# Performance work log

Hardware: AMD Instinct MI355X
Metric: run time of the kernel (lower is better)

Reference implementation:

```python
import jax, jax.numpy as jnp
import numpy as np

E = 768
H = 12
D = E // H  # 64


def setup_inputs() -> dict:
    key = jax.random.key(0)
    ks = jax.random.split(key, 12)
    B, S = 4, 2048
    scale = 1.0 / np.sqrt(E)
    inp = {
        "q": jax.random.normal(ks[0], (B, S, E), jnp.float32),
        "k": jax.random.normal(ks[1], (B, S, E), jnp.float32),
        "v": jax.random.normal(ks[2], (B, S, E), jnp.float32),
        "mask": jax.random.randint(ks[3], (B, S), 0, 2, jnp.int32),
        "Wq": jax.random.normal(ks[4], (E, E), jnp.float32) * scale,
        "bq": jnp.zeros((E,), jnp.float32),
        "Wk": jax.random.normal(ks[5], (E, E), jnp.float32) * scale,
        "bk": jnp.zeros((E,), jnp.float32),
        "Wv": jax.random.normal(ks[6], (E, E), jnp.float32) * scale,
        "bv": jnp.zeros((E,), jnp.float32),
        "Wo": jax.random.normal(ks[7], (E, E), jnp.float32) * scale,
        "bo": jnp.zeros((E,), jnp.float32),
    }
    return inp


def reference(q, k, v, mask, Wq, bq, Wk, bk, Wv, bv, Wo, bo):
    B, Sq, _ = q.shape
    Sk = k.shape[1]
    # QKV projections, split into heads: [B, H, S, D]
    qh = (q @ Wq + bq).reshape(B, Sq, H, D).transpose(0, 2, 1, 3)
    kh = (k @ Wk + bk).reshape(B, Sk, H, D).transpose(0, 2, 1, 3)
    vh = (v @ Wv + bv).reshape(B, Sk, H, D).transpose(0, 2, 1, 3)
    scores = jnp.einsum("bhqd,bhkd->bhqk", qh, kh) / jnp.sqrt(jnp.float32(D))
    # enc=True padding-mask path: positions where mask==0 get -1e9 added
    bias = jnp.where(mask == 0, jnp.float32(-1e9), jnp.float32(0.0))  # [B, Sk]
    scores = scores + bias[:, None, None, :]
    weights = jax.nn.softmax(scores, axis=-1)
    # dropout is identity in eval mode
    ctx = jnp.einsum("bhqk,bhkd->bqhd", weights, vh).reshape(B, Sq, E)
    return ctx @ Wo + bo
```

## Files before the change

kernel.cpp:

```cpp
#include <hip/hip_runtime.h>
#include <hip/hip_bf16.h>
#include <stdint.h>


typedef __bf16 bf16x8 __attribute__((ext_vector_type(8)));
typedef __bf16 bf16x4 __attribute__((ext_vector_type(4)));
typedef float floatx4 __attribute__((ext_vector_type(4)));

#define MFMA_BF16(a, b, c) __builtin_amdgcn_mfma_f32_16x16x32_bf16(a, b, c, 0, 0, 0)


__device__ __forceinline__ void glds16(const __bf16* g, __bf16* l) {
  __builtin_amdgcn_global_load_lds(
      (const __attribute__((address_space(1))) unsigned int*)g,
      (__attribute__((address_space(3))) unsigned int*)l, 16, 0, 0);
}

#if __has_builtin(__builtin_amdgcn_permlane32_swap)
__device__ __forceinline__ void perm32_swap(unsigned int& a, unsigned int& b) {
  auto r = __builtin_amdgcn_permlane32_swap(a, b, false, false);
  a = r[0];
  b = r[1];
}
#else
__device__ __forceinline__ void perm32_swap(unsigned int& a, unsigned int& b) {
  asm("v_permlane32_swap_b32 %0, %1" : "+v"(a), "+v"(b));
}
#endif

#if __has_builtin(__builtin_amdgcn_permlane16_swap)
__device__ __forceinline__ void perm16_swap(unsigned int& a, unsigned int& b) {
  auto r = __builtin_amdgcn_permlane16_swap(a, b, false, false);
  a = r[0];
  b = r[1];
}
#else
__device__ __forceinline__ void perm16_swap(unsigned int& a, unsigned int& b) {
  asm("v_permlane16_swap_b32 %0, %1" : "+v"(a), "+v"(b));
}
#endif

__global__ __launch_bounds__(256) void prep_transpose(
    const float* __restrict__ W0, const float* __restrict__ W1,
    const float* __restrict__ W2, const float* __restrict__ W3,
    __bf16* __restrict__ T0, __bf16* __restrict__ T1,
    __bf16* __restrict__ T2, __bf16* __restrict__ T3,
    const int* __restrict__ mask, float* __restrict__ biasF) {
  const int z = blockIdx.z;
  const float* W = (z == 0) ? W0 : (z == 1) ? W1 : (z == 2) ? W2 : W3;
  __bf16* T = (z == 0) ? T0 : (z == 1) ? T1 : (z == 2) ? T2 : T3;
  __shared__ float t[32][33];
  const int tx = threadIdx.x & 31, ty = threadIdx.x >> 5;
  const int kb = blockIdx.x * 32, nb = blockIdx.y * 32;
#pragma unroll
  for (int j = 0; j < 4; ++j)
    t[ty + j * 8][tx] = W[(size_t)(kb + ty + j * 8) * 768 + nb + tx];
  if (z == 3 && blockIdx.y == 0 && blockIdx.x < 8) {
    const int idx = blockIdx.x * 1024 + threadIdx.x * 4;
    const int4 m4 = *(const int4*)&mask[idx];
    float4 f4;
    f4.x = m4.x ? 0.0f : -1e5f;
    f4.y = m4.y ? 0.0f : -1e5f;
    f4.z = m4.z ? 0.0f : -1e5f;
    f4.w = m4.w ? 0.0f : -1e5f;
    *(float4*)&biasF[idx] = f4;
  }
  __syncthreads();
#pragma unroll
  for (int j = 0; j < 4; ++j)
    T[(size_t)(nb + ty + j * 8) * 768 + kb + tx] = (__bf16)t[tx][ty + j * 8];
}

__global__ __launch_bounds__(256) void qkv_gemm(
    const __bf16* __restrict__ Wtq, const __bf16* __restrict__ Wtk,
    const __bf16* __restrict__ Wtv, const float* __restrict__ Xq,
    const float* __restrict__ Xk, const float* __restrict__ Xv,
    const float* __restrict__ bq, const float* __restrict__ bk,
    const float* __restrict__ bv, __bf16* __restrict__ Qh,
    __bf16* __restrict__ Kh, __bf16* __restrict__ Vt) {
  __shared__ __align__(16) __bf16 As[2][128 * 32];
  __shared__ __align__(16) __bf16 Bs[2][128 * 32];
  const int gid = blockIdx.x + 6 * blockIdx.y + 384 * blockIdx.z;
  const int swz = (gid & 7) * 144 + (gid >> 3);
  const int z = swz / 384;
  const int rem = swz - z * 384;
  const int by = rem / 6;
  const int bx = rem - by * 6;

  const __bf16* Aop = (z == 0) ? Wtq : (z == 1) ? Wtk : Wtv;
  const float* Bop = (z == 0) ? Xq : (z == 1) ? Xk : Xv;
  const float* bias = (z == 0) ? bq : (z == 1) ? bk : bv;
  __bf16* Dst = (z == 0) ? Qh : (z == 1) ? Kh : Vt;
  const int m0 = bx * 128, n0 = by * 128;

  const int tid = threadIdx.x, lane = tid & 63, w = tid >> 6;
  const int quad = lane >> 4, l16 = lane & 15;
  const int wm = (w >> 1) * 64, wn = (w & 1) * 64;

  const int garow = w * 32 + (lane >> 2);
  const int gacol = (lane & 3) * 8;
  const __bf16* gA = Aop + (size_t)(m0 + garow) * 768 + gacol;
  const int brow = tid >> 3, bcol = (tid & 7) * 4;
  const float* gB = Bop + (size_t)(n0 + brow) * 768 + bcol;

  floatx4 acc[4][4] = {};
  float4 f[4];

  glds16(gA, &As[0][w * 1024]);
  glds16(gA + (size_t)16 * 768, &As[0][w * 1024 + 512]);
#pragma unroll
  for (int j = 0; j < 4; ++j) f[j] = *(const float4*)&gB[(size_t)(32 * j) * 768];
#pragma unroll
  for (int j = 0; j < 4; ++j) {
    bf16x4 pv;
    pv[0] = (__bf16)f[j].x; pv[1] = (__bf16)f[j].y;
    pv[2] = (__bf16)f[j].z; pv[3] = (__bf16)f[j].w;
    *(bf16x4*)&Bs[0][(brow + 32 * j) * 32 + bcol] = pv;
  }
#pragma unroll
  for (int j = 0; j < 4; ++j) f[j] = *(const float4*)&gB[(size_t)(32 * j) * 768 + 32];
  __syncthreads();

#pragma unroll 2
  for (int it = 0; it < 24; ++it) {
    const int c = it & 1;
    if (it < 23) {
      glds16(gA + (size_t)(it + 1) * 32, &As[c ^ 1][w * 1024]);
      glds16(gA + (size_t)(it + 1) * 32 + (size_t)16 * 768,
             &As[c ^ 1][w * 1024 + 512]);
    }
    bf16x8 af[4], bfr[4];
#pragma unroll
    for (int t = 0; t < 4; ++t) {
      af[t] = *(const bf16x8*)&As[c][(wm + t * 16 + l16) * 32 + quad * 8];
      bfr[t] = *(const bf16x8*)&Bs[c][(wn + t * 16 + l16) * 32 + quad * 8];
    }
    if (it < 23) {
#pragma unroll
      for (int j = 0; j < 4; ++j) {
        bf16x4 pv;
        pv[0] = (__bf16)f[j].x; pv[1] = (__bf16)f[j].y;
        pv[2] = (__bf16)f[j].z; pv[3] = (__bf16)f[j].w;
        *(bf16x4*)&Bs[c ^ 1][(brow + 32 * j) * 32 + bcol] = pv;
      }
    }
    if (it < 22) {
#pragma unroll
      for (int j = 0; j < 4; ++j)
        f[j] = *(const float4*)&gB[(size_t)(32 * j) * 768 + (it + 2) * 32];
    }
#pragma unroll
    for (int mt = 0; mt < 4; ++mt)
#pragma unroll
      for (int nt = 0; nt < 4; ++nt)
        acc[mt][nt] = MFMA_BF16(af[mt], bfr[nt], acc[mt][nt]);
    __syncthreads();
  }

  const float qs = (z == 0) ? 0.18033688011112042f : 1.0f;
#pragma unroll
  for (int mt = 0; mt < 4; ++mt) {
    const int e = m0 + wm + mt * 16 + quad * 4;
    const float4 b4 = *(const float4*)&bias[e];
    const int h = e >> 6, d = e & 63;
#pragma unroll
    for (int nt = 0; nt < 4; ++nt) {
      const int s = n0 + wn + nt * 16 + l16;
      const int bb = s >> 11, sr = s & 2047;
      const float v0 = (acc[mt][nt][0] + b4.x) * qs;
      const float v1 = (acc[mt][nt][1] + b4.y) * qs;
      const float v2 = (acc[mt][nt][2] + b4.z) * qs;
      const float v3 = (acc[mt][nt][3] + b4.w) * qs;
      if (z < 2) {
        bf16x4 pv;
        pv[0] = (__bf16)v0; pv[1] = (__bf16)v1; pv[2] = (__bf16)v2; pv[3] = (__bf16)v3;
        const int col = (z == 0) ? d : ((((d >> 3) ^ (sr & 7)) << 3) | (d & 7));
        *(bf16x4*)&Dst[((size_t)(bb * 12 + h) * 2048 + sr) * 64 + col] = pv;
      } else {
        const size_t rowbase = ((size_t)(bb * 12 + h) * 64 + d) * 2048;
        const int shi = sr & ~63, sblk = (sr >> 3) & 7, soff = sr & 7;
        Dst[rowbase + 0 * 2048 + shi + (((sblk ^ ((d + 0) & 7))) << 3) + soff] = (__bf16)v0;
        Dst[rowbase + 1 * 2048 + shi + (((sblk ^ ((d + 1) & 7))) << 3) + soff] = (__bf16)v1;
        Dst[rowbase + 2 * 2048 + shi + (((sblk ^ ((d + 2) & 7))) << 3) + soff] = (__bf16)v2;
        Dst[rowbase + 3 * 2048 + shi + (((sblk ^ ((d + 3) & 7))) << 3) + soff] = (__bf16)v3;
      }
    }
  }
}

__global__ __launch_bounds__(256) void out_gemm(const __bf16* __restrict__ Wto,
                                                const __bf16* __restrict__ Ctx,
                                                const float* __restrict__ bo,
                                                float* __restrict__ Out) {
  __shared__ __align__(16) __bf16 As[2][128 * 32];
  __shared__ __align__(16) __bf16 Bs[2][128 * 32];
  const int gid = blockIdx.x + 6 * blockIdx.y;
  const int swz = (gid & 7) * 48 + (gid >> 3);
  const int by = swz / 6;
  const int bx = swz - by * 6;
  const int m0 = bx * 128, n0 = by * 128;
  const int tid = threadIdx.x, lane = tid & 63, w = tid >> 6;
  const int quad = lane >> 4, l16 = lane & 15;
  const int wm = (w >> 1) * 64, wn = (w & 1) * 64;

  const int grow = w * 32 + (lane >> 2);
  const int gcol = (lane & 3) * 8;
  const __bf16* gA = Wto + (size_t)(m0 + grow) * 768 + gcol;
  const __bf16* gB = Ctx + (size_t)(n0 + grow) * 768 + gcol;

  floatx4 acc[4][4] = {};

  glds16(gA, &As[0][w * 1024]);
  glds16(gA + (size_t)16 * 768, &As[0][w * 1024 + 512]);
  glds16(gB, &Bs[0][w * 1024]);
  glds16(gB + (size_t)16 * 768, &Bs[0][w * 1024 + 512]);
  __syncthreads();

#pragma unroll 2
  for (int it = 0; it < 24; ++it) {
    const int c = it & 1;
    if (it < 23) {
      glds16(gA + (size_t)(it + 1) * 32, &As[c ^ 1][w * 1024]);
      glds16(gA + (size_t)(it + 1) * 32 + (size_t)16 * 768,
             &As[c ^ 1][w * 1024 + 512]);
      glds16(gB + (size_t)(it + 1) * 32, &Bs[c ^ 1][w * 1024]);
      glds16(gB + (size_t)(it + 1) * 32 + (size_t)16 * 768,
             &Bs[c ^ 1][w * 1024 + 512]);
    }
    bf16x8 af[4], bfr[4];
#pragma unroll
    for (int t = 0; t < 4; ++t) {
      af[t] = *(const bf16x8*)&As[c][(wm + t * 16 + l16) * 32 + quad * 8];
      bfr[t] = *(const bf16x8*)&Bs[c][(wn + t * 16 + l16) * 32 + quad * 8];
    }
#pragma unroll
    for (int mt = 0; mt < 4; ++mt)
#pragma unroll
      for (int nt = 0; nt < 4; ++nt)
        acc[mt][nt] = MFMA_BF16(af[mt], bfr[nt], acc[mt][nt]);
    __syncthreads();
  }

#pragma unroll
  for (int mt = 0; mt < 4; ++mt) {
    const int e = m0 + wm + mt * 16 + quad * 4;
    const float4 b4 = *(const float4*)&bo[e];
#pragma unroll
    for (int nt = 0; nt < 4; ++nt) {
      const int s = n0 + wn + nt * 16 + l16;
      float4 r;
      r.x = acc[mt][nt][0] + b4.x;
      r.y = acc[mt][nt][1] + b4.y;
      r.z = acc[mt][nt][2] + b4.z;
      r.w = acc[mt][nt][3] + b4.w;
      *(float4*)&Out[(size_t)s * 768 + e] = r;
    }
  }
}

__global__ __launch_bounds__(256) void attn_kernel(
    const __bf16* __restrict__ Qh, const __bf16* __restrict__ Kh,
    const __bf16* __restrict__ Vt, const float* __restrict__ biasF,
    __bf16* __restrict__ ctx) {
  const int lid = blockIdx.x + 16 * blockIdx.y;
  const int swz = (lid & 7) * 96 + (lid >> 3);
  const int qx = swz & 15, bh = swz >> 4;
  const int b = bh / 12, h = bh - b * 12;
  const int tid = threadIdx.x, lane = tid & 63, w = tid >> 6;
  const int quad = lane >> 4, l16 = lane & 15;
  const int q0 = qx * 128 + w * 32;

  __shared__ __align__(16) __bf16 Ks[2][64 * 64];
  __shared__ __align__(16) __bf16 Vs[2][64 * 64];

  const __bf16* Qbase = Qh + (size_t)bh * 2048 * 64;
  const __bf16* Kbase = Kh + (size_t)bh * 2048 * 64;
  const __bf16* Vbase = Vt + (size_t)bh * 64 * 2048;
  const float* biasB = biasF + b * 2048;

  bf16x8 bqf[2][2];
#pragma unroll
  for (int qt = 0; qt < 2; ++qt)
#pragma unroll
    for (int c = 0; c < 2; ++c)
      bqf[qt][c] =
          *(const bf16x8*)&Qbase[(size_t)(q0 + qt * 16 + l16) * 64 + c * 32 + quad * 8];

  const int r0 = (w * 2) * 8 + (lane >> 3);
  const int r1 = (w * 2 + 1) * 8 + (lane >> 3);
  const int scol = (lane & 7) * 8;
  const int d0 = (w * 2) * 512;
  const int d1 = (w * 2 + 1) * 512;
  const int col0 = (quad ^ (l16 & 7)) * 8;

  glds16(&Kbase[(size_t)r0 * 64 + scol], &Ks[0][d0]);
  glds16(&Kbase[(size_t)r1 * 64 + scol], &Ks[0][d1]);
  glds16(&Vbase[(size_t)r0 * 2048 + scol], &Vs[0][d0]);
  glds16(&Vbase[(size_t)r1 * 2048 + scol], &Vs[0][d1]);

  floatx4 o[4][2] = {};
  floatx4 os[2] = {};
  bf16x8 ones8;
#pragma unroll
  for (int j = 0; j < 8; ++j) ones8[j] = (__bf16)1.0f;

  for (int it = 0; it < 32; ++it) {
    const int kt = it * 64;
    const int cur = it & 1;
    const int nxt = cur ^ 1;
    const int nkt = (kt + 64) & 2047;

    __syncthreads();

    glds16(&Kbase[(size_t)(nkt + r0) * 64 + scol], &Ks[nxt][d0]);
    glds16(&Kbase[(size_t)(nkt + r1) * 64 + scol], &Ks[nxt][d1]);
    glds16(&Vbase[(size_t)r0 * 2048 + nkt + scol], &Vs[nxt][d0]);
    glds16(&Vbase[(size_t)r1 * 2048 + nkt + scol], &Vs[nxt][d1]);

    floatx4 sc[4][2];
#pragma unroll
    for (int t = 0; t < 4; ++t) {
      const float4 bf4 = *(const float4*)&biasB[kt + t * 16 + quad * 4];
      bf16x8 ak0 = *(const bf16x8*)&Ks[cur][(t * 16 + l16) * 64 + col0];
      bf16x8 ak1 = *(const bf16x8*)&Ks[cur][(t * 16 + l16) * 64 + (col0 ^ 32)];
#pragma unroll
      for (int qt = 0; qt < 2; ++qt) {
        floatx4 zz;
        zz[0] = bf4.x; zz[1] = bf4.y; zz[2] = bf4.z; zz[3] = bf4.w;
        zz = MFMA_BF16(ak0, bqf[qt][0], zz);
        zz = MFMA_BF16(ak1, bqf[qt][1], zz);
        sc[t][qt] = zz;
      }
    }
    unsigned int u[4][2][2];
#pragma unroll
    for (int t = 0; t < 4; ++t)
#pragma unroll
      for (int qt = 0; qt < 2; ++qt) {
        const float e0 = __builtin_amdgcn_exp2f(sc[t][qt][0]);
        const float e1 = __builtin_amdgcn_exp2f(sc[t][qt][1]);
        const float e2 = __builtin_amdgcn_exp2f(sc[t][qt][2]);
        const float e3 = __builtin_amdgcn_exp2f(sc[t][qt][3]);
        asm("v_cvt_pk_bf16_f32 %0, %1, %2" : "=v"(u[t][qt][0]) : "v"(e0), "v"(e1));
        asm("v_cvt_pk_bf16_f32 %0, %1, %2" : "=v"(u[t][qt][1]) : "v"(e2), "v"(e3));
      }
#pragma unroll
    for (int c = 0; c < 2; ++c) {
      bf16x8 bp[2];
#pragma unroll
      for (int qt = 0; qt < 2; ++qt) {
        unsigned int w0 = u[2 * c][qt][0], w1 = u[2 * c][qt][1];
        unsigned int w2 = u[2 * c + 1][qt][0], w3 = u[2 * c + 1][qt][1];
        perm32_swap(w0, w2);
        perm32_swap(w1, w3);
        perm16_swap(w0, w2);
        perm16_swap(w1, w3);
        union { unsigned int wd[4]; bf16x8 v; } ub;
        ub.wd[0] = w0; ub.wd[1] = w1; ub.wd[2] = w2; ub.wd[3] = w3;
        bp[qt] = ub.v;
        os[qt] = MFMA_BF16(ones8, bp[qt], os[qt]);
      }
#pragma unroll
      for (int dt = 0; dt < 4; ++dt) {
        bf16x8 av = *(const bf16x8*)&Vs[cur][(dt * 16 + l16) * 64 + (col0 ^ (c * 32))];
#pragma unroll
        for (int qt = 0; qt < 2; ++qt) o[dt][qt] = MFMA_BF16(av, bp[qt], o[dt][qt]);
      }
    }
  }

  float inv[2];
  inv[0] = 1.0f / os[0][0];
  inv[1] = 1.0f / os[1][0];
#pragma unroll
  for (int dt = 0; dt < 4; ++dt)
#pragma unroll
    for (int qt = 0; qt < 2; ++qt) {
      const int q = q0 + qt * 16 + l16;
      const int d = h * 64 + dt * 16 + quad * 4;
      bf16x4 pv;
      pv[0] = (__bf16)(o[dt][qt][0] * inv[qt]);
      pv[1] = (__bf16)(o[dt][qt][1] * inv[qt]);
      pv[2] = (__bf16)(o[dt][qt][2] * inv[qt]);
      pv[3] = (__bf16)(o[dt][qt][3] * inv[qt]);
      *(bf16x4*)&ctx[(size_t)(b * 2048 + q) * 768 + d] = pv;
    }
}

extern "C" void kernel_launch(void* const* d_in, const int* in_sizes, int n_in,
                              void* d_out, int out_size, void* d_ws, size_t ws_size,
                              hipStream_t stream) {
  const float* q = (const float*)d_in[0];
  const float* k = (const float*)d_in[1];
  const float* v = (const float*)d_in[2];
  const int* mask = (const int*)d_in[3];
  const float* Wq = (const float*)d_in[4];
  const float* bq = (const float*)d_in[5];
  const float* Wk = (const float*)d_in[6];
  const float* bk = (const float*)d_in[7];
  const float* Wv = (const float*)d_in[8];
  const float* bv = (const float*)d_in[9];
  const float* Wo = (const float*)d_in[10];
  const float* bo = (const float*)d_in[11];
  float* out = (float*)d_out;

  char* ws = (char*)d_ws;
  const size_t SZ = (size_t)8192 * 768 * 2;
  const size_t WSZ = (size_t)768 * 768 * 2;
  __bf16* Qh = (__bf16*)(ws);
  __bf16* Kh = (__bf16*)(ws + SZ);
  __bf16* Vt = (__bf16*)(ws + 2 * SZ);
  __bf16* ctx = (__bf16*)(ws + 3 * SZ);
  __bf16* Wtq = (__bf16*)(ws + 4 * SZ);
  __bf16* Wtk = (__bf16*)(ws + 4 * SZ + WSZ);
  __bf16* Wtv = (__bf16*)(ws + 4 * SZ + 2 * WSZ);
  __bf16* Wto = (__bf16*)(ws + 4 * SZ + 3 * WSZ);
  float* biasF = (float*)(ws + 4 * SZ + 4 * WSZ);

  prep_transpose<<<dim3(24, 24, 4), 256, 0, stream>>>(Wq, Wk, Wv, Wo, Wtq, Wtk,
                                                      Wtv, Wto, mask, biasF);
  qkv_gemm<<<dim3(6, 64, 3), 256, 0, stream>>>(Wtq, Wtk, Wtv, q, k, v, bq, bk, bv,
                                               Qh, Kh, Vt);
  attn_kernel<<<dim3(16, 48), 256, 0, stream>>>(Qh, Kh, Vt, biasF, ctx);
  out_gemm<<<dim3(6, 64), 256, 0, stream>>>(Wto, ctx, bo, out);
}
```

Before: 300.5 us.

## Pre-convert activations to bf16 and stream both GEMM operands via LDS-direct loads

```diff
diff --git a/kernel.cpp b/kernel.cpp
--- a/kernel.cpp
+++ b/kernel.cpp
@@ -71,10 +71,27 @@
     T[(size_t)(nb + ty + j * 8) * 768 + kb + tx] = (__bf16)t[tx][ty + j * 8];
 }
 
+__global__ __launch_bounds__(256) void xcvt(
+    const float* __restrict__ X0, const float* __restrict__ X1,
+    const float* __restrict__ X2, __bf16* __restrict__ Y0,
+    __bf16* __restrict__ Y1, __bf16* __restrict__ Y2) {
+  const int z = blockIdx.y;
+  const float* X = (z == 0) ? X0 : (z == 1) ? X1 : X2;
+  __bf16* Y = (z == 0) ? Y0 : (z == 1) ? Y1 : Y2;
+  const size_t i = ((size_t)blockIdx.x * 256 + threadIdx.x) * 8;
+  const float4 a = *(const float4*)&X[i];
+  const float4 b = *(const float4*)&X[i + 4];
+  bf16x4 p0, p1;
+  p0[0] = (__bf16)a.x; p0[1] = (__bf16)a.y; p0[2] = (__bf16)a.z; p0[3] = (__bf16)a.w;
+  p1[0] = (__bf16)b.x; p1[1] = (__bf16)b.y; p1[2] = (__bf16)b.z; p1[3] = (__bf16)b.w;
+  *(bf16x4*)&Y[i] = p0;
+  *(bf16x4*)&Y[i + 4] = p1;
+}
+
 __global__ __launch_bounds__(256) void qkv_gemm(
     const __bf16* __restrict__ Wtq, const __bf16* __restrict__ Wtk,
-    const __bf16* __restrict__ Wtv, const float* __restrict__ Xq,
-    const float* __restrict__ Xk, const float* __restrict__ Xv,
+    const __bf16* __restrict__ Wtv, const __bf16* __restrict__ Xbq,
+    const __bf16* __restrict__ Xbk, const __bf16* __restrict__ Xbv,
     const float* __restrict__ bq, const float* __restrict__ bk,
     const float* __restrict__ bv, __bf16* __restrict__ Qh,
     __bf16* __restrict__ Kh, __bf16* __restrict__ Vt) {
@@ -88,7 +105,7 @@
   const int bx = rem - by * 6;
 
   const __bf16* Aop = (z == 0) ? Wtq : (z == 1) ? Wtk : Wtv;
-  const float* Bop = (z == 0) ? Xq : (z == 1) ? Xk : Xv;
+  const __bf16* Bop = (z == 0) ? Xbq : (z == 1) ? Xbk : Xbv;
   const float* bias = (z == 0) ? bq : (z == 1) ? bk : bv;
   __bf16* Dst = (z == 0) ? Qh : (z == 1) ? Kh : Vt;
   const int m0 = bx * 128, n0 = by * 128;
@@ -97,37 +114,29 @@
   const int quad = lane >> 4, l16 = lane & 15;
   const int wm = (w >> 1) * 64, wn = (w & 1) * 64;
 
-  const int garow = w * 32 + (lane >> 2);
-  const int gacol = (lane & 3) * 8;
-  const __bf16* gA = Aop + (size_t)(m0 + garow) * 768 + gacol;
-  const int brow = tid >> 3, bcol = (tid & 7) * 4;
-  const float* gB = Bop + (size_t)(n0 + brow) * 768 + bcol;
+  const int grow = w * 32 + (lane >> 2);
+  const int gcol = (lane & 3) * 8;
+  const __bf16* gA = Aop + (size_t)(m0 + grow) * 768 + gcol;
+  const __bf16* gB = Bop + (size_t)(n0 + grow) * 768 + gcol;
 
   floatx4 acc[4][4] = {};
-  float4 f[4];
 
   glds16(gA, &As[0][w * 1024]);
   glds16(gA + (size_t)16 * 768, &As[0][w * 1024 + 512]);
-#pragma unroll
-  for (int j = 0; j < 4; ++j) f[j] = *(const float4*)&gB[(size_t)(32 * j) * 768];
-#pragma unroll
-  for (int j = 0; j < 4; ++j) {
-    bf16x4 pv;
-    pv[0] = (__bf16)f[j].x; pv[1] = (__bf16)f[j].y;
-    pv[2] = (__bf16)f[j].z; pv[3] = (__bf16)f[j].w;
-    *(bf16x4*)&Bs[0][(brow + 32 * j) * 32 + bcol] = pv;
-  }
-#pragma unroll
-  for (int j = 0; j < 4; ++j) f[j] = *(const float4*)&gB[(size_t)(32 * j) * 768 + 32];
-  __syncthreads();
+  glds16(gB, &Bs[0][w * 1024]);
+  glds16(gB + (size_t)16 * 768, &Bs[0][w * 1024 + 512]);
 
 #pragma unroll 2
   for (int it = 0; it < 24; ++it) {
     const int c = it & 1;
+    __syncthreads();
     if (it < 23) {
       glds16(gA + (size_t)(it + 1) * 32, &As[c ^ 1][w * 1024]);
       glds16(gA + (size_t)(it + 1) * 32 + (size_t)16 * 768,
              &As[c ^ 1][w * 1024 + 512]);
+      glds16(gB + (size_t)(it + 1) * 32, &Bs[c ^ 1][w * 1024]);
+      glds16(gB + (size_t)(it + 1) * 32 + (size_t)16 * 768,
+             &Bs[c ^ 1][w * 1024 + 512]);
     }
     bf16x8 af[4], bfr[4];
 #pragma unroll
@@ -135,26 +144,11 @@
       af[t] = *(const bf16x8*)&As[c][(wm + t * 16 + l16) * 32 + quad * 8];
       bfr[t] = *(const bf16x8*)&Bs[c][(wn + t * 16 + l16) * 32 + quad * 8];
     }
-    if (it < 23) {
-#pragma unroll
-      for (int j = 0; j < 4; ++j) {
-        bf16x4 pv;
-        pv[0] = (__bf16)f[j].x; pv[1] = (__bf16)f[j].y;
-        pv[2] = (__bf16)f[j].z; pv[3] = (__bf16)f[j].w;
-        *(bf16x4*)&Bs[c ^ 1][(brow + 32 * j) * 32 + bcol] = pv;
-      }
-    }
-    if (it < 22) {
-#pragma unroll
-      for (int j = 0; j < 4; ++j)
-        f[j] = *(const float4*)&gB[(size_t)(32 * j) * 768 + (it + 2) * 32];
-    }
 #pragma unroll
     for (int mt = 0; mt < 4; ++mt)
 #pragma unroll
       for (int nt = 0; nt < 4; ++nt)
         acc[mt][nt] = MFMA_BF16(af[mt], bfr[nt], acc[mt][nt]);
-    __syncthreads();
   }
 
   const float qs = (z == 0) ? 0.18033688011112042f : 1.0f;
@@ -214,11 +208,11 @@
   glds16(gA + (size_t)16 * 768, &As[0][w * 1024 + 512]);
   glds16(gB, &Bs[0][w * 1024]);
   glds16(gB + (size_t)16 * 768, &Bs[0][w * 1024 + 512]);
-  __syncthreads();
 
 #pragma unroll 2
   for (int it = 0; it < 24; ++it) {
     const int c = it & 1;
+    __syncthreads();
     if (it < 23) {
       glds16(gA + (size_t)(it + 1) * 32, &As[c ^ 1][w * 1024]);
       glds16(gA + (size_t)(it + 1) * 32 + (size_t)16 * 768,
@@ -238,7 +232,6 @@
 #pragma unroll
       for (int nt = 0; nt < 4; ++nt)
         acc[mt][nt] = MFMA_BF16(af[mt], bfr[nt], acc[mt][nt]);
-    __syncthreads();
   }
 
 #pragma unroll
@@ -411,16 +404,20 @@
   __bf16* Kh = (__bf16*)(ws + SZ);
   __bf16* Vt = (__bf16*)(ws + 2 * SZ);
   __bf16* ctx = (__bf16*)(ws + 3 * SZ);
-  __bf16* Wtq = (__bf16*)(ws + 4 * SZ);
-  __bf16* Wtk = (__bf16*)(ws + 4 * SZ + WSZ);
-  __bf16* Wtv = (__bf16*)(ws + 4 * SZ + 2 * WSZ);
-  __bf16* Wto = (__bf16*)(ws + 4 * SZ + 3 * WSZ);
-  float* biasF = (float*)(ws + 4 * SZ + 4 * WSZ);
+  __bf16* Xbq = ctx;
+  __bf16* Xbk = (__bf16*)(ws + 4 * SZ);
+  __bf16* Xbv = (__bf16*)(ws + 5 * SZ);
+  __bf16* Wtq = (__bf16*)(ws + 6 * SZ);
+  __bf16* Wtk = (__bf16*)(ws + 6 * SZ + WSZ);
+  __bf16* Wtv = (__bf16*)(ws + 6 * SZ + 2 * WSZ);
+  __bf16* Wto = (__bf16*)(ws + 6 * SZ + 3 * WSZ);
+  float* biasF = (float*)(ws + 6 * SZ + 4 * WSZ);
 
   prep_transpose<<<dim3(24, 24, 4), 256, 0, stream>>>(Wq, Wk, Wv, Wo, Wtq, Wtk,
                                                       Wtv, Wto, mask, biasF);
-  qkv_gemm<<<dim3(6, 64, 3), 256, 0, stream>>>(Wtq, Wtk, Wtv, q, k, v, bq, bk, bv,
-                                               Qh, Kh, Vt);
+  xcvt<<<dim3(3072, 3), 256, 0, stream>>>(q, k, v, Xbq, Xbk, Xbv);
+  qkv_gemm<<<dim3(6, 64, 3), 256, 0, stream>>>(Wtq, Wtk, Wtv, Xbq, Xbk, Xbv,
+                                               bq, bk, bv, Qh, Kh, Vt);
   attn_kernel<<<dim3(16, 48), 256, 0, stream>>>(Qh, Kh, Vt, biasF, ctx);
   out_gemm<<<dim3(6, 64), 256, 0, stream>>>(Wto, ctx, bo, out);
 }
```

New measurement: 285.1 us. 1.05x faster.
